# Performance work log

Hardware: AMD Instinct MI355X
Metric: run time of the kernel (lower is better)

Reference implementation:

```python
import jax, jax.numpy as jnp
import numpy as np

V_IPC, N_ROLES, D = 50000, 16, 256
B, L = 2048, 64
F_BIB, H1, H2, D_OUT = 512, 1024, 1024, 512
N_EXP, N_CLS = 8, 10
LN_EPS = 1e-5


def setup_inputs() -> dict:
    key = jax.random.key(0)
    ks = jax.random.split(key, 24)
    s = 0.05
    ipc_emb = jax.random.normal(ks[0], (V_IPC, D), jnp.float32) * s
    ipc_emb = ipc_emb.at[0].set(0.0)  # padding_idx=0
    role_emb = jax.random.normal(ks[1], (N_ROLES, D), jnp.float32) * s
    role_emb = role_emb.at[0].set(0.0)
    inp = {
        "ipc_indices": jax.random.randint(ks[2], (B, L), 0, V_IPC),
        "role_indices": jax.random.randint(ks[3], (B, L), 0, N_ROLES),
        "bibliometric_features": jax.random.normal(ks[4], (B, F_BIB), jnp.float32),
        "ipc_padding_mask": jax.random.randint(ks[5], (B, L), 0, 2).astype(jnp.int32),
        "top_k": 2,
        "ipc_emb": ipc_emb,
        "role_emb": role_emb,
        "Wq": jax.random.normal(ks[6], (D, D), jnp.float32) * s,
        "bq": jnp.zeros((D,), jnp.float32),
        "Wk": jax.random.normal(ks[7], (D, D), jnp.float32) * s,
        "bk": jnp.zeros((D,), jnp.float32),
        "Wv": jax.random.normal(ks[8], (D, D), jnp.float32) * s,
        "bv": jnp.zeros((D,), jnp.float32),
        "global_context": jax.random.normal(ks[9], (D,), jnp.float32) * s,
        "ln_g": jnp.ones((D,), jnp.float32),
        "ln_b": jnp.zeros((D,), jnp.float32),
        "gate_W": jax.random.normal(ks[10], (D, N_EXP), jnp.float32) * s,
        "gate_b": jnp.zeros((N_EXP,), jnp.float32),
        "expert_biases": jnp.zeros((N_EXP,), jnp.float32),
        "W1": jax.random.normal(ks[11], (N_EXP, F_BIB, H1), jnp.float32) * s,
        "b1": jnp.zeros((N_EXP, H1), jnp.float32),
        "W2": jax.random.normal(ks[12], (N_EXP, H1, H2), jnp.float32) * s,
        "b2": jnp.zeros((N_EXP, H2), jnp.float32),
        "W3": jax.random.normal(ks[13], (N_EXP, H2, D_OUT), jnp.float32) * s,
        "b3": jnp.zeros((N_EXP, D_OUT), jnp.float32),
        "head_W": jax.random.normal(ks[14], (D_OUT, N_CLS), jnp.float32) * s,
        "head_b": jnp.zeros((N_CLS,), jnp.float32),
    }
    return inp


def reference(ipc_indices, role_indices, bibliometric_features, ipc_padding_mask, top_k,
              ipc_emb, role_emb, Wq, bq, Wk, bk, Wv, bv, global_context, ln_g, ln_b,
              gate_W, gate_b, expert_biases, W1, b1, W2, b2, W3, b3, head_W, head_b):
    # embeddings + role combine  -> [B, L, D]
    x = ipc_emb[ipc_indices] + role_emb[role_indices]
    # attention pooling with a global learned query (same query for every batch row)
    keys = x @ Wk + bk                                  # [B, L, D]
    values = x @ Wv + bv                                # [B, L, D]
    q = global_context @ Wq + bq                        # [D]
    scores = jnp.einsum('d,bld->bl', q, keys)           # [B, L]
    scores = jnp.where(ipc_padding_mask == 0, -1e9, scores)
    attn = jax.nn.softmax(scores, axis=-1)              # [B, L]
    pooled = jnp.einsum('bl,bld->bd', attn, values)     # [B, D]
    mu = pooled.mean(-1, keepdims=True)
    var = ((pooled - mu) ** 2).mean(-1, keepdims=True)
    router_in = (pooled - mu) / jnp.sqrt(var + LN_EPS) * ln_g + ln_b
    # router: select with biased scores, gate with unbiased scores
    affinity = router_in @ gate_W + gate_b              # [B, E]
    sel_scores = affinity + expert_biases
    _, idx = jax.lax.top_k(sel_scores, top_k)           # [B, K]
    gw = jax.nn.softmax(jnp.take_along_axis(affinity, idx, axis=-1), axis=-1)  # [B, K]
    # dense all-expert MLP (reference form of masked per-expert loop)
    h = jax.nn.relu(jnp.einsum('bi,eih->ebh', bibliometric_features, W1) + b1[:, None, :])
    h = jax.nn.relu(jnp.einsum('ebh,ehj->ebj', h, W2) + b2[:, None, :])
    eo = jnp.einsum('ebj,ejo->ebo', h, W3) + b3[:, None, :]  # [E, B, O]
    # gather each token's top-k expert outputs and combine
    bidx = jnp.arange(idx.shape[0])[:, None]            # [B, 1]
    sel_out = eo[idx, bidx]                             # [B, K, O]
    moe_out = jnp.einsum('bk,bko->bo', gw, sel_out)     # [B, O]
    logits = moe_out @ head_W + head_b                  # [B, n_classes]
    return logits, idx
```

## Files before the change

### kernel.cpp

```cpp
#include <hip/hip_runtime.h>
#include <hip/hip_bf16.h>
#include <math.h>


#define LN_EPS 1e-5f

typedef __bf16 bf16_t;
typedef __bf16 bf16x8 __attribute__((ext_vector_type(8)));
typedef float f32x4 __attribute__((ext_vector_type(4)));

__device__ __forceinline__ void async_ld16(const void* g, void* l) {
  __builtin_amdgcn_global_load_lds(
      (__attribute__((address_space(1))) void*)g,
      (__attribute__((address_space(3))) void*)l, 16, 0, 0);
}

__global__ __launch_bounds__(256)
void prep_kq(const float* __restrict__ Wq, const float* __restrict__ bq,
             const float* __restrict__ Wk, const float* __restrict__ bk,
             const float* __restrict__ gc, float* __restrict__ kq_out) {
  __shared__ float q[256];
  __shared__ float red[4];
  const int t = threadIdx.x, bi = blockIdx.x;
  float s = bq[t];
  for (int d = 0; d < 256; d++) s += gc[d] * Wq[d * 256 + t];
  q[t] = s;
  __syncthreads();
  const int rl = t >> 5, sl = t & 31;
  const int r = bi * 8 + rl;
  float p = 0.f;
#pragma unroll
  for (int i = 0; i < 8; i++) { const int d = sl + 32 * i; p += Wk[r * 256 + d] * q[d]; }
#pragma unroll
  for (int o = 16; o > 0; o >>= 1) p += __shfl_down(p, o, 32);
  if (sl == 0) kq_out[r] = p;
  if (bi == 0) {
    float z = q[t] * bk[t];
    const int lane = t & 63, wave = t >> 6;
#pragma unroll
    for (int o = 32; o > 0; o >>= 1) z += __shfl_down(z, o);
    if (lane == 0) red[wave] = z;
    __syncthreads();
    if (t == 0) kq_out[256] = red[0] + red[1] + red[2] + red[3];
  }
}

__global__ __launch_bounds__(256)
void transpose_conv(const float* __restrict__ W, bf16_t* __restrict__ Wt,
                    int R, int C) {
  __shared__ float tile[32][33];
  const int e = blockIdx.z;
  const int c0 = blockIdx.x * 32, r0 = blockIdx.y * 32;
  const int tx = threadIdx.x & 31, ty = threadIdx.x >> 5;
  const float* Wp = W + (size_t)e * R * C;
  bf16_t* Wtp = Wt + (size_t)e * R * C;
#pragma unroll
  for (int i = 0; i < 4; i++)
    tile[ty + 8 * i][tx] = Wp[(size_t)(r0 + ty + 8 * i) * C + (c0 + tx)];
  __syncthreads();
#pragma unroll
  for (int i = 0; i < 4; i++)
    Wtp[(size_t)(c0 + ty + 8 * i) * R + (r0 + tx)] = (bf16_t)tile[tx][ty + 8 * i];
}

__global__ __launch_bounds__(256)
void router_kernel(const int* __restrict__ ipc_idx, const int* __restrict__ role_idx,
                   const int* __restrict__ maskp,
                   const float* __restrict__ ipc_emb, const float* __restrict__ role_emb,
                   const float* __restrict__ kq_qbk,
                   const float* __restrict__ Wv, const float* __restrict__ bvec,
                   const float* __restrict__ ln_g, const float* __restrict__ ln_b,
                   const float* __restrict__ gate_W, const float* __restrict__ gate_b,
                   const float* __restrict__ expert_biases,
                   float* __restrict__ out_idx_f, int* __restrict__ ws_idx,
                   float* __restrict__ ws_gw) {
  const int b = blockIdx.x;
  __shared__ float sc[64];
  __shared__ float attn_s[64];
  __shared__ __align__(16) float part[4][256];
  __shared__ float xbar[256];
  __shared__ float rv[256];
  __shared__ float red[4];
  __shared__ float aff[8];
  const int t = threadIdx.x, wave = t >> 6, lane = t & 63;
  const int d0 = lane * 4;
  const float4 kq = *(const float4*)(kq_qbk + d0);
  const float qbk = kq_qbk[256];

  for (int l = wave; l < 64; l += 4) {
    const int ii = ipc_idx[b * 64 + l], ri = role_idx[b * 64 + l];
    const float4 xe = *(const float4*)(ipc_emb + (size_t)ii * 256 + d0);
    const float4 re = *(const float4*)(role_emb + (size_t)ri * 256 + d0);
    float p = (xe.x + re.x) * kq.x + (xe.y + re.y) * kq.y +
              (xe.z + re.z) * kq.z + (xe.w + re.w) * kq.w;
#pragma unroll
    for (int o = 32; o > 0; o >>= 1) p += __shfl_down(p, o);
    if (lane == 0) sc[l] = (maskp[b * 64 + l] == 0) ? -1e9f : (p + qbk);
  }
  __syncthreads();
  if (wave == 0) {
    const float s = sc[lane];
    float m = s;
#pragma unroll
    for (int o = 32; o > 0; o >>= 1) m = fmaxf(m, __shfl_xor(m, o));
    const float ev = expf(s - m);
    float sum = ev;
#pragma unroll
    for (int o = 32; o > 0; o >>= 1) sum += __shfl_xor(sum, o);
    attn_s[lane] = ev / sum;
  }
  __syncthreads();
  float p0 = 0.f, p1 = 0.f, p2 = 0.f, p3 = 0.f;
  for (int l = wave; l < 64; l += 4) {
    const float a = attn_s[l];
    const int ii = ipc_idx[b * 64 + l], ri = role_idx[b * 64 + l];
    const float4 xe = *(const float4*)(ipc_emb + (size_t)ii * 256 + d0);
    const float4 re = *(const float4*)(role_emb + (size_t)ri * 256 + d0);
    p0 += a * (xe.x + re.x); p1 += a * (xe.y + re.y);
    p2 += a * (xe.z + re.z); p3 += a * (xe.w + re.w);
  }
  *(float4*)&part[wave][d0] = make_float4(p0, p1, p2, p3);
  __syncthreads();
  xbar[t] = part[0][t] + part[1][t] + part[2][t] + part[3][t];
  __syncthreads();
  float pv = bvec[t];
  for (int d = 0; d < 256; d++) pv += xbar[d] * Wv[d * 256 + t];
  float s1 = pv;
#pragma unroll
  for (int o = 32; o > 0; o >>= 1) s1 += __shfl_down(s1, o);
  if (lane == 0) red[wave] = s1;
  __syncthreads();
  const float mu = (red[0] + red[1] + red[2] + red[3]) * (1.f / 256.f);
  __syncthreads();
  const float df = pv - mu;
  float s2 = df * df;
#pragma unroll
  for (int o = 32; o > 0; o >>= 1) s2 += __shfl_down(s2, o);
  if (lane == 0) red[wave] = s2;
  __syncthreads();
  const float var = (red[0] + red[1] + red[2] + red[3]) * (1.f / 256.f);
  rv[t] = df / sqrtf(var + LN_EPS) * ln_g[t] + ln_b[t];
  __syncthreads();
  if (wave == 0) {
    const int j = lane & 7, dbase = (lane >> 3) * 32;
    float p = 0.f;
    for (int i = 0; i < 32; i++) p += rv[dbase + i] * gate_W[(dbase + i) * 8 + j];
    p += __shfl_xor(p, 8); p += __shfl_xor(p, 16); p += __shfl_xor(p, 32);
    if (lane < 8) aff[j] = p + gate_b[j];
  }
  __syncthreads();
  if (t == 0) {
    float b0 = -1e30f; int i0 = 0;
    for (int j = 0; j < 8; j++) {
      const float s = aff[j] + expert_biases[j];
      if (s > b0) { b0 = s; i0 = j; }
    }
    float b1v = -1e30f; int i1 = 0;
    for (int j = 0; j < 8; j++) {
      if (j == i0) continue;
      const float s = aff[j] + expert_biases[j];
      if (s > b1v) { b1v = s; i1 = j; }
    }
    const float a0 = aff[i0], a1 = aff[i1];
    const float m = fmaxf(a0, a1);
    const float e0 = expf(a0 - m), e1 = expf(a1 - m);
    const float inv = 1.f / (e0 + e1);
    ws_idx[b * 2] = i0; ws_idx[b * 2 + 1] = i1;
    ws_gw[b * 2] = e0 * inv; ws_gw[b * 2 + 1] = e1 * inv;
    out_idx_f[b * 2] = (float)i0; out_idx_f[b * 2 + 1] = (float)i1;
  }
}

__global__ __launch_bounds__(256)
void pack_kernel(const int* __restrict__ ws_idx, int* __restrict__ list_token,
                 int* __restrict__ a_of, int* __restrict__ offsets_g) {
  __shared__ int cnt[8]; __shared__ int off[9]; __shared__ int fill[8];
  const int t = threadIdx.x;
  if (t < 8) cnt[t] = 0;
  __syncthreads();
  for (int a = t; a < 4096; a += 256) atomicAdd(&cnt[ws_idx[a]], 1);
  __syncthreads();
  if (t == 0) { off[0] = 0; for (int e = 0; e < 8; e++) off[e + 1] = off[e] + cnt[e]; }
  __syncthreads();
  if (t < 8) fill[t] = off[t];
  if (t < 9) offsets_g[t] = off[t];
  __syncthreads();
  for (int a = t; a < 4096; a += 256) {
    const int e = ws_idx[a];
    const int pos = atomicAdd(&fill[e], 1);
    list_token[pos] = a >> 1;
    a_of[a] = pos;
  }
}

__global__ __launch_bounds__(64)
void gather_bib(const float* __restrict__ bib, const int* __restrict__ list_token,
                bf16_t* __restrict__ Xc) {
  const int a = blockIdx.x;
  const int tok = list_token[a];
  const int t = threadIdx.x;
  const float4 v1 = *(const float4*)(bib + (size_t)tok * 512 + t * 8);
  const float4 v2 = *(const float4*)(bib + (size_t)tok * 512 + t * 8 + 4);
  bf16x8 o;
  o[0] = (bf16_t)v1.x; o[1] = (bf16_t)v1.y; o[2] = (bf16_t)v1.z; o[3] = (bf16_t)v1.w;
  o[4] = (bf16_t)v2.x; o[5] = (bf16_t)v2.y; o[6] = (bf16_t)v2.z; o[7] = (bf16_t)v2.w;
  *(bf16x8*)(Xc + (size_t)a * 512 + t * 8) = o;
}

template <bool RELU, typename OUT_T>
__global__ __launch_bounds__(256)
void expert_gemm(const bf16_t* __restrict__ A, const bf16_t* __restrict__ Bt,
                 const float* __restrict__ bias, OUT_T* __restrict__ C,
                 const int* __restrict__ offsets, int K, int N) {
  const int e = blockIdx.z;
  const int seg_hi = offsets[e + 1];
  const int row0 = offsets[e] + blockIdx.y * 128;
  if (row0 >= seg_hi) return;
  const int n0 = blockIdx.x * 128;
  __shared__ __align__(16) bf16_t As[128 * 32];
  __shared__ __align__(16) bf16_t Bs[128 * 32];
  const int t = threadIdx.x;
  const int wave = t >> 6, lane = t & 63;
  const int wm = wave >> 1, wn = wave & 1;
  const bf16_t* Ab = A + (size_t)row0 * K;
  const bf16_t* Bb = Bt + ((size_t)e * N + n0) * K;
  const int r0s = (wave * 2 + 0) * 16 + (lane >> 2);
  const int r1s = (wave * 2 + 1) * 16 + (lane >> 2);
  const int kg = (lane & 3) * 8;
  bf16_t* la0 = As + (wave * 2 + 0) * 512 + lane * 8;
  bf16_t* la1 = As + (wave * 2 + 1) * 512 + lane * 8;
  bf16_t* lb0 = Bs + (wave * 2 + 0) * 512 + lane * 8;
  bf16_t* lb1 = Bs + (wave * 2 + 1) * 512 + lane * 8;
  f32x4 acc[4][4];
#pragma unroll
  for (int i = 0; i < 4; i++)
#pragma unroll
    for (int j = 0; j < 4; j++) acc[i][j] = (f32x4){0.f, 0.f, 0.f, 0.f};
  const int fr = lane & 15, fq = (lane >> 4) * 8;
  for (int kk = 0; kk < K; kk += 32) {
    async_ld16(Ab + (size_t)r0s * K + kk + kg, la0);
    async_ld16(Ab + (size_t)r1s * K + kk + kg, la1);
    async_ld16(Bb + (size_t)r0s * K + kk + kg, lb0);
    async_ld16(Bb + (size_t)r1s * K + kk + kg, lb1);
    __syncthreads();
    bf16x8 af[4], bfv[4];
#pragma unroll
    for (int mi = 0; mi < 4; mi++)
      af[mi] = *(const bf16x8*)(As + (wm * 64 + mi * 16 + fr) * 32 + fq);
#pragma unroll
    for (int ni = 0; ni < 4; ni++)
      bfv[ni] = *(const bf16x8*)(Bs + (wn * 64 + ni * 16 + fr) * 32 + fq);
    __syncthreads();
#pragma unroll
    for (int mi = 0; mi < 4; mi++)
#pragma unroll
      for (int ni = 0; ni < 4; ni++)
        acc[mi][ni] = __builtin_amdgcn_mfma_f32_16x16x32_bf16(af[mi], bfv[ni], acc[mi][ni], 0, 0, 0);
  }
#pragma unroll
  for (int ni = 0; ni < 4; ni++) {
    const int col = n0 + wn * 64 + ni * 16 + fr;
    const float bv = bias[e * N + col];
#pragma unroll
    for (int mi = 0; mi < 4; mi++) {
#pragma unroll
      for (int r = 0; r < 4; r++) {
        const int grow = row0 + wm * 64 + mi * 16 + (lane >> 4) * 4 + r;
        if (grow < seg_hi) {
          float v = acc[mi][ni][r] + bv;
          if (RELU) v = fmaxf(v, 0.f);
          C[(size_t)grow * N + col] = (OUT_T)v;
        }
      }
    }
  }
}

__global__ __launch_bounds__(256)
void head_kernel(const float* __restrict__ O, const int* __restrict__ a_of,
                 const float* __restrict__ ws_gw, const float* __restrict__ head_W,
                 const float* __restrict__ head_b, float* __restrict__ out) {
  const int b = blockIdx.x, t = threadIdx.x;
  __shared__ float m[512];
  const int a0 = a_of[b * 2], a1 = a_of[b * 2 + 1];
  const float g0 = ws_gw[b * 2], g1 = ws_gw[b * 2 + 1];
  for (int d = t; d < 512; d += 256)
    m[d] = g0 * O[(size_t)a0 * 512 + d] + g1 * O[(size_t)a1 * 512 + d];
  __syncthreads();
  if (t < 160) {
    const int c = t >> 4, ch = t & 15;
    float p = 0.f;
#pragma unroll
    for (int i = 0; i < 32; i++) {
      const int d = i * 16 + ch;
      p += m[d] * head_W[d * 10 + c];
    }
#pragma unroll
    for (int o = 8; o > 0; o >>= 1) p += __shfl_down(p, o, 16);
    if (ch == 0) out[b * 10 + c] = p + head_b[c];
  }
}

extern "C" void kernel_launch(void* const* d_in, const int* in_sizes, int n_in,
                              void* d_out, int out_size, void* d_ws, size_t ws_size,
                              hipStream_t stream) {
  const int* ipc_idx = (const int*)d_in[0];
  const int* role_idx = (const int*)d_in[1];
  const float* bib = (const float*)d_in[2];
  const int* maskp = (const int*)d_in[3];
  const float* ipc_emb = (const float*)d_in[5];
  const float* role_emb = (const float*)d_in[6];
  const float* Wq = (const float*)d_in[7];
  const float* bq = (const float*)d_in[8];
  const float* Wk = (const float*)d_in[9];
  const float* bk = (const float*)d_in[10];
  const float* Wv = (const float*)d_in[11];
  const float* bv = (const float*)d_in[12];
  const float* gc = (const float*)d_in[13];
  const float* ln_g = (const float*)d_in[14];
  const float* ln_b = (const float*)d_in[15];
  const float* gate_W = (const float*)d_in[16];
  const float* gate_b = (const float*)d_in[17];
  const float* exp_b = (const float*)d_in[18];
  const float* W1 = (const float*)d_in[19];
  const float* b1 = (const float*)d_in[20];
  const float* W2 = (const float*)d_in[21];
  const float* b2 = (const float*)d_in[22];
  const float* W3 = (const float*)d_in[23];
  const float* b3 = (const float*)d_in[24];
  const float* head_W = (const float*)d_in[25];
  const float* head_b = (const float*)d_in[26];

  char* ws = (char*)d_ws;
  size_t off = 0;
  auto alloc = [&](size_t bytes) -> char* {
    char* p = ws + off;
    off += (bytes + 255) & ~(size_t)255;
    return p;
  };
  float* kq_qbk = (float*)alloc(257 * 4);
  int* ws_idx = (int*)alloc(4096 * 4);
  float* ws_gw = (float*)alloc(4096 * 4);
  int* list_tok = (int*)alloc(4096 * 4);
  int* a_of = (int*)alloc(4096 * 4);
  int* offs = (int*)alloc(9 * 4);
  bf16_t* W1t = (bf16_t*)alloc((size_t)8 * 1024 * 512 * 2);
  bf16_t* W2t = (bf16_t*)alloc((size_t)8 * 1024 * 1024 * 2);
  bf16_t* W3t = (bf16_t*)alloc((size_t)8 * 512 * 1024 * 2);
  bf16_t* Xc = (bf16_t*)alloc((size_t)4224 * 512 * 2);
  bf16_t* H1c = (bf16_t*)alloc((size_t)4224 * 1024 * 2);
  bf16_t* H2c = (bf16_t*)alloc((size_t)4224 * 1024 * 2);
  float* Oc = (float*)alloc((size_t)4224 * 512 * 4);
  (void)in_sizes; (void)n_in; (void)out_size; (void)ws_size;

  float* out_logits = (float*)d_out;
  float* out_idx = (float*)d_out + 20480;

  prep_kq<<<32, 256, 0, stream>>>(Wq, bq, Wk, bk, gc, kq_qbk);
  transpose_conv<<<dim3(1024 / 32, 512 / 32, 8), 256, 0, stream>>>(W1, W1t, 512, 1024);
  transpose_conv<<<dim3(1024 / 32, 1024 / 32, 8), 256, 0, stream>>>(W2, W2t, 1024, 1024);
  transpose_conv<<<dim3(512 / 32, 1024 / 32, 8), 256, 0, stream>>>(W3, W3t, 1024, 512);
  router_kernel<<<2048, 256, 0, stream>>>(ipc_idx, role_idx, maskp, ipc_emb, role_emb,
                                          kq_qbk, Wv, bv, ln_g, ln_b, gate_W, gate_b,
                                          exp_b, out_idx, ws_idx, ws_gw);
  pack_kernel<<<1, 256, 0, stream>>>(ws_idx, list_tok, a_of, offs);
  gather_bib<<<4096, 64, 0, stream>>>(bib, list_tok, Xc);
  expert_gemm<true, bf16_t><<<dim3(8, 16, 8), 256, 0, stream>>>(Xc, W1t, b1, H1c, offs, 512, 1024);
  expert_gemm<true, bf16_t><<<dim3(8, 16, 8), 256, 0, stream>>>(H1c, W2t, b2, H2c, offs, 1024, 1024);
  expert_gemm<false, float><<<dim3(4, 16, 8), 256, 0, stream>>>(H2c, W3t, b3, Oc, offs, 1024, 512);
  head_kernel<<<2048, 256, 0, stream>>>(Oc, a_of, ws_gw, head_W, head_b, out_logits);
}
```

Before: 394.0 us.

## Precompute embedding score table, split router, widen transpose, retile expert GEMMs

The attention score is now precomputed per vocabulary row as a 50016-entry table, so the router no longer gathers embeddings twice for scoring. The router is split into an xbar kernel and a batched pool kernel that handles 8 rows per block for the Wv projection, LayerNorm and gating. The weight transpose uses 64x64 tiles with vectorized loads and stores. Expert GEMMs take templated smaller tiles (64xN) to launch more blocks. The cost is an extra pass over the full 50k embedding table plus more kernel launches and intermediate buffers.

```diff
diff --git a/kernel.cpp b/kernel.cpp
--- a/kernel.cpp
+++ b/kernel.cpp
@@ -7,6 +7,7 @@
 
 typedef __bf16 bf16_t;
 typedef __bf16 bf16x8 __attribute__((ext_vector_type(8)));
+typedef __bf16 bf16x4 __attribute__((ext_vector_type(4)));
 typedef float f32x4 __attribute__((ext_vector_type(4)));
 
 __device__ __forceinline__ void async_ld16(const void* g, void* l) {
@@ -46,60 +47,64 @@
 }
 
 __global__ __launch_bounds__(256)
-void transpose_conv(const float* __restrict__ W, bf16_t* __restrict__ Wt,
-                    int R, int C) {
-  __shared__ float tile[32][33];
+void transpose64(const float* __restrict__ W, bf16_t* __restrict__ Wt,
+                 int R, int C) {
+  __shared__ float tile[64][65];
   const int e = blockIdx.z;
-  const int c0 = blockIdx.x * 32, r0 = blockIdx.y * 32;
-  const int tx = threadIdx.x & 31, ty = threadIdx.x >> 5;
+  const int c0 = blockIdx.x * 64, r0 = blockIdx.y * 64;
+  const int tq = threadIdx.x & 15, th = threadIdx.x >> 4;
   const float* Wp = W + (size_t)e * R * C;
   bf16_t* Wtp = Wt + (size_t)e * R * C;
 #pragma unroll
-  for (int i = 0; i < 4; i++)
-    tile[ty + 8 * i][tx] = Wp[(size_t)(r0 + ty + 8 * i) * C + (c0 + tx)];
-  __syncthreads();
-#pragma unroll
-  for (int i = 0; i < 4; i++)
-    Wtp[(size_t)(c0 + ty + 8 * i) * R + (r0 + tx)] = (bf16_t)tile[tx][ty + 8 * i];
-}
-
-__global__ __launch_bounds__(256)
-void router_kernel(const int* __restrict__ ipc_idx, const int* __restrict__ role_idx,
-                   const int* __restrict__ maskp,
-                   const float* __restrict__ ipc_emb, const float* __restrict__ role_emb,
-                   const float* __restrict__ kq_qbk,
-                   const float* __restrict__ Wv, const float* __restrict__ bvec,
-                   const float* __restrict__ ln_g, const float* __restrict__ ln_b,
-                   const float* __restrict__ gate_W, const float* __restrict__ gate_b,
-                   const float* __restrict__ expert_biases,
-                   float* __restrict__ out_idx_f, int* __restrict__ ws_idx,
-                   float* __restrict__ ws_gw) {
+  for (int i = 0; i < 4; i++) {
+    const int row = th + 16 * i;
+    *(float4*)&tile[row][tq * 4] = *(const float4*)(Wp + (size_t)(r0 + row) * C + c0 + tq * 4);
+  }
+  __syncthreads();
+#pragma unroll
+  for (int i = 0; i < 4; i++) {
+    const int c_loc = th + 16 * i;
+    bf16x4 o;
+#pragma unroll
+    for (int j = 0; j < 4; j++) o[j] = (bf16_t)tile[tq * 4 + j][c_loc];
+    *(bf16x4*)(Wtp + (size_t)(c0 + c_loc) * R + r0 + tq * 4) = o;
+  }
+}
+
+__global__ __launch_bounds__(256)
+void score_tab_kernel(const float* __restrict__ ipc_emb,
+                      const float* __restrict__ role_emb,
+                      const float* __restrict__ kq_qbk, float* __restrict__ tab) {
+  const int wave = threadIdx.x >> 6, lane = threadIdx.x & 63;
+  const float4 kq = *(const float4*)(kq_qbk + lane * 4);
+  const int base = (blockIdx.x * 4 + wave) * 32;
+  for (int i = 0; i < 32; i++) {
+    const int r = base + i;
+    if (r >= 50016) return;
+    const float* src = (r < 50000) ? (ipc_emb + (size_t)r * 256)
+                                   : (role_emb + (size_t)(r - 50000) * 256);
+    const float4 v = *(const float4*)(src + lane * 4);
+    float p = v.x * kq.x + v.y * kq.y + v.z * kq.z + v.w * kq.w;
+#pragma unroll
+    for (int o = 32; o > 0; o >>= 1) p += __shfl_down(p, o);
+    if (lane == 0) tab[r] = (r < 50000) ? p : (p + kq_qbk[256]);
+  }
+}
+
+__global__ __launch_bounds__(256)
+void xbar_kernel(const int* __restrict__ ipc_idx, const int* __restrict__ role_idx,
+                 const int* __restrict__ maskp,
+                 const float* __restrict__ ipc_emb, const float* __restrict__ role_emb,
+                 const float* __restrict__ tab, float* __restrict__ xbar_g) {
   const int b = blockIdx.x;
-  __shared__ float sc[64];
   __shared__ float attn_s[64];
   __shared__ __align__(16) float part[4][256];
-  __shared__ float xbar[256];
-  __shared__ float rv[256];
-  __shared__ float red[4];
-  __shared__ float aff[8];
   const int t = threadIdx.x, wave = t >> 6, lane = t & 63;
   const int d0 = lane * 4;
-  const float4 kq = *(const float4*)(kq_qbk + d0);
-  const float qbk = kq_qbk[256];
-
-  for (int l = wave; l < 64; l += 4) {
-    const int ii = ipc_idx[b * 64 + l], ri = role_idx[b * 64 + l];
-    const float4 xe = *(const float4*)(ipc_emb + (size_t)ii * 256 + d0);
-    const float4 re = *(const float4*)(role_emb + (size_t)ri * 256 + d0);
-    float p = (xe.x + re.x) * kq.x + (xe.y + re.y) * kq.y +
-              (xe.z + re.z) * kq.z + (xe.w + re.w) * kq.w;
-#pragma unroll
-    for (int o = 32; o > 0; o >>= 1) p += __shfl_down(p, o);
-    if (lane == 0) sc[l] = (maskp[b * 64 + l] == 0) ? -1e9f : (p + qbk);
-  }
-  __syncthreads();
   if (wave == 0) {
-    const float s = sc[lane];
+    const int ii = ipc_idx[b * 64 + lane], ri = role_idx[b * 64 + lane];
+    float s = tab[ii] + tab[50000 + ri];
+    s = (maskp[b * 64 + lane] == 0) ? -1e9f : s;
     float m = s;
 #pragma unroll
     for (int o = 32; o > 0; o >>= 1) m = fmaxf(m, __shfl_xor(m, o));
@@ -121,53 +126,103 @@
   }
   *(float4*)&part[wave][d0] = make_float4(p0, p1, p2, p3);
   __syncthreads();
-  xbar[t] = part[0][t] + part[1][t] + part[2][t] + part[3][t];
-  __syncthreads();
-  float pv = bvec[t];
-  for (int d = 0; d < 256; d++) pv += xbar[d] * Wv[d * 256 + t];
-  float s1 = pv;
-#pragma unroll
-  for (int o = 32; o > 0; o >>= 1) s1 += __shfl_down(s1, o);
-  if (lane == 0) red[wave] = s1;
-  __syncthreads();
-  const float mu = (red[0] + red[1] + red[2] + red[3]) * (1.f / 256.f);
-  __syncthreads();
-  const float df = pv - mu;
-  float s2 = df * df;
-#pragma unroll
-  for (int o = 32; o > 0; o >>= 1) s2 += __shfl_down(s2, o);
-  if (lane == 0) red[wave] = s2;
-  __syncthreads();
-  const float var = (red[0] + red[1] + red[2] + red[3]) * (1.f / 256.f);
-  rv[t] = df / sqrtf(var + LN_EPS) * ln_g[t] + ln_b[t];
-  __syncthreads();
-  if (wave == 0) {
-    const int j = lane & 7, dbase = (lane >> 3) * 32;
-    float p = 0.f;
-    for (int i = 0; i < 32; i++) p += rv[dbase + i] * gate_W[(dbase + i) * 8 + j];
-    p += __shfl_xor(p, 8); p += __shfl_xor(p, 16); p += __shfl_xor(p, 32);
-    if (lane < 8) aff[j] = p + gate_b[j];
-  }
-  __syncthreads();
-  if (t == 0) {
-    float b0 = -1e30f; int i0 = 0;
-    for (int j = 0; j < 8; j++) {
-      const float s = aff[j] + expert_biases[j];
-      if (s > b0) { b0 = s; i0 = j; }
-    }
-    float b1v = -1e30f; int i1 = 0;
-    for (int j = 0; j < 8; j++) {
-      if (j == i0) continue;
-      const float s = aff[j] + expert_biases[j];
-      if (s > b1v) { b1v = s; i1 = j; }
-    }
-    const float a0 = aff[i0], a1 = aff[i1];
-    const float m = fmaxf(a0, a1);
-    const float e0 = expf(a0 - m), e1 = expf(a1 - m);
-    const float inv = 1.f / (e0 + e1);
-    ws_idx[b * 2] = i0; ws_idx[b * 2 + 1] = i1;
-    ws_gw[b * 2] = e0 * inv; ws_gw[b * 2 + 1] = e1 * inv;
-    out_idx_f[b * 2] = (float)i0; out_idx_f[b * 2 + 1] = (float)i1;
+  xbar_g[(size_t)b * 256 + t] = part[0][t] + part[1][t] + part[2][t] + part[3][t];
+}
+
+__global__ __launch_bounds__(256)
+void pool_kernel(const float* __restrict__ xbar_g, const float* __restrict__ Wv,
+                 const float* __restrict__ bvec,
+                 const float* __restrict__ ln_g, const float* __restrict__ ln_b,
+                 const float* __restrict__ gate_W, const float* __restrict__ gate_b,
+                 const float* __restrict__ expert_biases,
+                 float* __restrict__ out_idx_f, int* __restrict__ ws_idx,
+                 float* __restrict__ ws_gw) {
+  const int rb = blockIdx.x * 8;
+  __shared__ __align__(16) float xs[8][256];
+  __shared__ __align__(16) float ps[8][260];
+  const int t = threadIdx.x, wave = t >> 6, lane = t & 63;
+  for (int i = t; i < 512; i += 256)
+    ((float4*)xs)[i] = ((const float4*)(xbar_g + (size_t)rb * 256))[i];
+  __syncthreads();
+  const float* x0 = xs[wave * 2];
+  const float* x1 = xs[wave * 2 + 1];
+  f32x4 acc0 = {0.f, 0.f, 0.f, 0.f}, acc1 = {0.f, 0.f, 0.f, 0.f};
+  for (int d = 0; d < 256; d += 4) {
+    const float4 xa = *(const float4*)(x0 + d);
+    const float4 xb = *(const float4*)(x1 + d);
+#pragma unroll
+    for (int j = 0; j < 4; j++) {
+      const float4 wv = *(const float4*)(Wv + (size_t)(d + j) * 256 + lane * 4);
+      const float aj = (&xa.x)[j], bj = (&xb.x)[j];
+      acc0.x += aj * wv.x; acc0.y += aj * wv.y; acc0.z += aj * wv.z; acc0.w += aj * wv.w;
+      acc1.x += bj * wv.x; acc1.y += bj * wv.y; acc1.z += bj * wv.z; acc1.w += bj * wv.w;
+    }
+  }
+  const float4 bvv = *(const float4*)(bvec + lane * 4);
+  acc0.x += bvv.x; acc0.y += bvv.y; acc0.z += bvv.z; acc0.w += bvv.w;
+  acc1.x += bvv.x; acc1.y += bvv.y; acc1.z += bvv.z; acc1.w += bvv.w;
+  *(f32x4*)&ps[wave * 2][lane * 4] = acc0;
+  *(f32x4*)&ps[wave * 2 + 1][lane * 4] = acc1;
+  __syncthreads();
+  const float4 lg = *(const float4*)(ln_g + lane * 4);
+  const float4 lb = *(const float4*)(ln_b + lane * 4);
+#pragma unroll
+  for (int rr = 0; rr < 2; rr++) {
+    const int r = wave * 2 + rr;
+    const float4 v = *(const float4*)&ps[r][lane * 4];
+    float s1 = v.x + v.y + v.z + v.w;
+#pragma unroll
+    for (int o = 32; o > 0; o >>= 1) s1 += __shfl_xor(s1, o);
+    const float mu = s1 * (1.f / 256.f);
+    const float4 df = make_float4(v.x - mu, v.y - mu, v.z - mu, v.w - mu);
+    float s2 = df.x * df.x + df.y * df.y + df.z * df.z + df.w * df.w;
+#pragma unroll
+    for (int o = 32; o > 0; o >>= 1) s2 += __shfl_xor(s2, o);
+    const float inv = 1.f / sqrtf(s2 * (1.f / 256.f) + LN_EPS);
+    f32x4 rv;
+    rv[0] = df.x * inv * lg.x + lb.x; rv[1] = df.y * inv * lg.y + lb.y;
+    rv[2] = df.z * inv * lg.z + lb.z; rv[3] = df.w * inv * lg.w + lb.w;
+    f32x4 pa = {0.f, 0.f, 0.f, 0.f}, pb = {0.f, 0.f, 0.f, 0.f};
+#pragma unroll
+    for (int k = 0; k < 4; k++) {
+      const int d = lane * 4 + k;
+      const f32x4 g0 = *(const f32x4*)(gate_W + d * 8);
+      const f32x4 g1 = *(const f32x4*)(gate_W + d * 8 + 4);
+      pa += rv[k] * g0;
+      pb += rv[k] * g1;
+    }
+#pragma unroll
+    for (int o = 32; o > 0; o >>= 1) {
+      pa[0] += __shfl_down(pa[0], o); pa[1] += __shfl_down(pa[1], o);
+      pa[2] += __shfl_down(pa[2], o); pa[3] += __shfl_down(pa[3], o);
+      pb[0] += __shfl_down(pb[0], o); pb[1] += __shfl_down(pb[1], o);
+      pb[2] += __shfl_down(pb[2], o); pb[3] += __shfl_down(pb[3], o);
+    }
+    if (lane == 0) {
+      float aff[8];
+#pragma unroll
+      for (int j = 0; j < 4; j++) { aff[j] = pa[j] + gate_b[j]; aff[4 + j] = pb[j] + gate_b[4 + j]; }
+      float b0 = -1e30f; int i0 = 0;
+#pragma unroll
+      for (int j = 0; j < 8; j++) {
+        const float s = aff[j] + expert_biases[j];
+        if (s > b0) { b0 = s; i0 = j; }
+      }
+      float b1v = -1e30f; int i1 = 0;
+#pragma unroll
+      for (int j = 0; j < 8; j++) {
+        const float s = aff[j] + expert_biases[j];
+        if (j != i0 && s > b1v) { b1v = s; i1 = j; }
+      }
+      const float a0 = aff[i0], a1 = aff[i1];
+      const float m = fmaxf(a0, a1);
+      const float e0 = expf(a0 - m), e1 = expf(a1 - m);
+      const float invs = 1.f / (e0 + e1);
+      const int bg = rb + r;
+      ws_idx[bg * 2] = i0; ws_idx[bg * 2 + 1] = i1;
+      ws_gw[bg * 2] = e0 * invs; ws_gw[bg * 2 + 1] = e1 * invs;
+      out_idx_f[bg * 2] = (float)i0; out_idx_f[bg * 2 + 1] = (float)i1;
+    }
   }
 }
 
@@ -207,69 +262,70 @@
   *(bf16x8*)(Xc + (size_t)a * 512 + t * 8) = o;
 }
 
-template <bool RELU, typename OUT_T>
+template <bool RELU, typename OUT_T, int MI, int NI>
 __global__ __launch_bounds__(256)
 void expert_gemm(const bf16_t* __restrict__ A, const bf16_t* __restrict__ Bt,
                  const float* __restrict__ bias, OUT_T* __restrict__ C,
-                 const int* __restrict__ offsets, int K, int N) {
+                 const int* __restrict__ offsets, int K, int Nt) {
+  constexpr int M = MI * 32, N = NI * 32;
   const int e = blockIdx.z;
   const int seg_hi = offsets[e + 1];
-  const int row0 = offsets[e] + blockIdx.y * 128;
+  const int row0 = offsets[e] + blockIdx.y * M;
   if (row0 >= seg_hi) return;
-  const int n0 = blockIdx.x * 128;
-  __shared__ __align__(16) bf16_t As[128 * 32];
-  __shared__ __align__(16) bf16_t Bs[128 * 32];
+  const int n0 = blockIdx.x * N;
+  __shared__ __align__(16) bf16_t As[M * 32];
+  __shared__ __align__(16) bf16_t Bs[N * 32];
   const int t = threadIdx.x;
   const int wave = t >> 6, lane = t & 63;
   const int wm = wave >> 1, wn = wave & 1;
   const bf16_t* Ab = A + (size_t)row0 * K;
-  const bf16_t* Bb = Bt + ((size_t)e * N + n0) * K;
-  const int r0s = (wave * 2 + 0) * 16 + (lane >> 2);
-  const int r1s = (wave * 2 + 1) * 16 + (lane >> 2);
-  const int kg = (lane & 3) * 8;
-  bf16_t* la0 = As + (wave * 2 + 0) * 512 + lane * 8;
-  bf16_t* la1 = As + (wave * 2 + 1) * 512 + lane * 8;
-  bf16_t* lb0 = Bs + (wave * 2 + 0) * 512 + lane * 8;
-  bf16_t* lb1 = Bs + (wave * 2 + 1) * 512 + lane * 8;
-  f32x4 acc[4][4];
-#pragma unroll
-  for (int i = 0; i < 4; i++)
-#pragma unroll
-    for (int j = 0; j < 4; j++) acc[i][j] = (f32x4){0.f, 0.f, 0.f, 0.f};
+  const bf16_t* Bb = Bt + ((size_t)e * Nt + n0) * K;
+  const int rowA = lane >> 2, kg = (lane & 3) * 8;
+  f32x4 acc[MI][NI];
+#pragma unroll
+  for (int i = 0; i < MI; i++)
+#pragma unroll
+    for (int j = 0; j < NI; j++) acc[i][j] = (f32x4){0.f, 0.f, 0.f, 0.f};
   const int fr = lane & 15, fq = (lane >> 4) * 8;
   for (int kk = 0; kk < K; kk += 32) {
-    async_ld16(Ab + (size_t)r0s * K + kk + kg, la0);
-    async_ld16(Ab + (size_t)r1s * K + kk + kg, la1);
-    async_ld16(Bb + (size_t)r0s * K + kk + kg, lb0);
-    async_ld16(Bb + (size_t)r1s * K + kk + kg, lb1);
+#pragma unroll
+    for (int j = 0; j < M / 64; j++) {
+      const int r = (wave * (M / 64) + j) * 16;
+      async_ld16(Ab + (size_t)(r + rowA) * K + kk + kg, As + r * 32 + lane * 8);
+    }
+#pragma unroll
+    for (int j = 0; j < N / 64; j++) {
+      const int r = (wave * (N / 64) + j) * 16;
+      async_ld16(Bb + (size_t)(r + rowA) * K + kk + kg, Bs + r * 32 + lane * 8);
+    }
     __syncthreads();
-    bf16x8 af[4], bfv[4];
-#pragma unroll
-    for (int mi = 0; mi < 4; mi++)
-      af[mi] = *(const bf16x8*)(As + (wm * 64 + mi * 16 + fr) * 32 + fq);
-#pragma unroll
-    for (int ni = 0; ni < 4; ni++)
-      bfv[ni] = *(const bf16x8*)(Bs + (wn * 64 + ni * 16 + fr) * 32 + fq);
+    bf16x8 af[MI], bfv[NI];
+#pragma unroll
+    for (int mi = 0; mi < MI; mi++)
+      af[mi] = *(const bf16x8*)(As + (wm * MI * 16 + mi * 16 + fr) * 32 + fq);
+#pragma unroll
+    for (int ni = 0; ni < NI; ni++)
+      bfv[ni] = *(const bf16x8*)(Bs + (wn * NI * 16 + ni * 16 + fr) * 32 + fq);
     __syncthreads();
 #pragma unroll
-    for (int mi = 0; mi < 4; mi++)
-#pragma unroll
-      for (int ni = 0; ni < 4; ni++)
+    for (int mi = 0; mi < MI; mi++)
+#pragma unroll
+      for (int ni = 0; ni < NI; ni++)
         acc[mi][ni] = __builtin_amdgcn_mfma_f32_16x16x32_bf16(af[mi], bfv[ni], acc[mi][ni], 0, 0, 0);
   }
 #pragma unroll
-  for (int ni = 0; ni < 4; ni++) {
-    const int col = n0 + wn * 64 + ni * 16 + fr;
-    const float bv = bias[e * N + col];
-#pragma unroll
-    for (int mi = 0; mi < 4; mi++) {
+  for (int ni = 0; ni < NI; ni++) {
+    const int col = n0 + wn * NI * 16 + ni * 16 + fr;
+    const float bv = bias[e * Nt + col];
+#pragma unroll
+    for (int mi = 0; mi < MI; mi++) {
 #pragma unroll
       for (int r = 0; r < 4; r++) {
-        const int grow = row0 + wm * 64 + mi * 16 + (lane >> 4) * 4 + r;
+        const int grow = row0 + wm * MI * 16 + mi * 16 + (lane >> 4) * 4 + r;
         if (grow < seg_hi) {
           float v = acc[mi][ni][r] + bv;
           if (RELU) v = fmaxf(v, 0.f);
-          C[(size_t)grow * N + col] = (OUT_T)v;
+          C[(size_t)grow * Nt + col] = (OUT_T)v;
         }
       }
     }
@@ -339,6 +395,8 @@
     return p;
   };
   float* kq_qbk = (float*)alloc(257 * 4);
+  float* tab = (float*)alloc(50016 * 4);
+  float* xbar_g = (float*)alloc((size_t)2048 * 256 * 4);
   int* ws_idx = (int*)alloc(4096 * 4);
   float* ws_gw = (float*)alloc(4096 * 4);
   int* list_tok = (int*)alloc(4096 * 4);
@@ -357,16 +415,18 @@
   float* out_idx = (float*)d_out + 20480;
 
   prep_kq<<<32, 256, 0, stream>>>(Wq, bq, Wk, bk, gc, kq_qbk);
-  transpose_conv<<<dim3(1024 / 32, 512 / 32, 8), 256, 0, stream>>>(W1, W1t, 512, 1024);
-  transpose_conv<<<dim3(1024 / 32, 1024 / 32, 8), 256, 0, stream>>>(W2, W2t, 1024, 1024);
-  transpose_conv<<<dim3(512 / 32, 1024 / 32, 8), 256, 0, stream>>>(W3, W3t, 1024, 512);
-  router_kernel<<<2048, 256, 0, stream>>>(ipc_idx, role_idx, maskp, ipc_emb, role_emb,
-                                          kq_qbk, Wv, bv, ln_g, ln_b, gate_W, gate_b,
-                                          exp_b, out_idx, ws_idx, ws_gw);
+  transpose64<<<dim3(1024 / 64, 512 / 64, 8), 256, 0, stream>>>(W1, W1t, 512, 1024);
+  transpose64<<<dim3(1024 / 64, 1024 / 64, 8), 256, 0, stream>>>(W2, W2t, 1024, 1024);
+  transpose64<<<dim3(512 / 64, 1024 / 64, 8), 256, 0, stream>>>(W3, W3t, 1024, 512);
+  score_tab_kernel<<<391, 256, 0, stream>>>(ipc_emb, role_emb, kq_qbk, tab);
+  xbar_kernel<<<2048, 256, 0, stream>>>(ipc_idx, role_idx, maskp, ipc_emb, role_emb,
+                                        tab, xbar_g);
+  pool_kernel<<<256, 256, 0, stream>>>(xbar_g, Wv, bv, ln_g, ln_b, gate_W, gate_b,
+                                       exp_b, out_idx, ws_idx, ws_gw);
   pack_kernel<<<1, 256, 0, stream>>>(ws_idx, list_tok, a_of, offs);
   gather_bib<<<4096, 64, 0, stream>>>(bib, list_tok, Xc);
-  expert_gemm<true, bf16_t><<<dim3(8, 16, 8), 256, 0, stream>>>(Xc, W1t, b1, H1c, offs, 512, 1024);
-  expert_gemm<true, bf16_t><<<dim3(8, 16, 8), 256, 0, stream>>>(H1c, W2t, b2, H2c, offs, 1024, 1024);
-  expert_gemm<false, float><<<dim3(4, 16, 8), 256, 0, stream>>>(H2c, W3t, b3, Oc, offs, 1024, 512);
+  expert_gemm<true, bf16_t, 2, 4><<<dim3(8, 32, 8), 256, 0, stream>>>(Xc, W1t, b1, H1c, offs, 512, 1024);
+  expert_gemm<true, bf16_t, 2, 4><<<dim3(8, 32, 8), 256, 0, stream>>>(H1c, W2t, b2, H2c, offs, 1024, 1024);
+  expert_gemm<false, float, 2, 2><<<dim3(8, 32, 8), 256, 0, stream>>>(H2c, W3t, b3, Oc, offs, 1024, 512);
   head_kernel<<<2048, 256, 0, stream>>>(Oc, a_of, ws_gw, head_W, head_b, out_logits);
 }
```

Result: slower. 411.6 us (+4.5%).
